# Performance work log

Measured on AMD Instinct MI355X. Metric: run time of the kernel, lower is better.

Reference implementation:

```python
import jax, jax.numpy as jnp
import numpy as np

BN_EPS = 1e-5
TAU = 1.0  # gumbel temperature

def setup_inputs() -> dict:
    key = jax.random.key(0)
    ks = jax.random.split(key, 6)
    B, O, F, H, HID = 32, 4096, 256, 8, 128
    x = jax.random.normal(ks[0], (B, O, F), dtype=jnp.float32)
    gumbel_noise = jax.random.gumbel(ks[1], (B, O, H), dtype=jnp.float32)
    W_in = jax.random.normal(ks[2], (F, HID), dtype=jnp.float32) * (1.0 / np.sqrt(F))
    b_in = jnp.zeros((HID,), jnp.float32)
    W_blk = jax.random.normal(ks[3], (HID, HID), dtype=jnp.float32) * (1.0 / np.sqrt(HID))
    b_blk = jnp.zeros((HID,), jnp.float32)
    bn_gamma = jnp.ones((HID,), jnp.float32)
    bn_beta = jnp.zeros((HID,), jnp.float32)
    W_fc = jax.random.normal(ks[4], (HID, H), dtype=jnp.float32) * (1.0 / np.sqrt(HID))
    b_fc = jnp.zeros((H,), jnp.float32)
    return {"x": x, "gumbel_noise": gumbel_noise, "W_in": W_in, "b_in": b_in,
            "W_blk": W_blk, "b_blk": b_blk, "bn_gamma": bn_gamma, "bn_beta": bn_beta,
            "W_fc": W_fc, "b_fc": b_fc}

def reference(x, gumbel_noise, W_in, b_in, W_blk, b_blk, bn_gamma, bn_beta, W_fc, b_fc):
    B, O, F = x.shape
    xf = x.reshape(B * O, F)
    # DynamicNetwork head: input linear + relu, one residual block (Linear+BN+ReLU), fc
    h = jax.nn.relu(xf @ W_in + b_in)  # (B*O, HID)
    z = h @ W_blk + b_blk
    mu = z.mean(axis=0)
    var = z.var(axis=0)  # biased var, matches BatchNorm training normalization
    z = (z - mu) * jax.lax.rsqrt(var + BN_EPS) * bn_gamma + bn_beta
    h = jax.nn.relu(z) + h  # residual
    logits = (h @ W_fc + b_fc).reshape(B, O, -1)  # (B, O, H)
    # mask out zero-norm observations
    mask = (jnp.linalg.norm(x, axis=2) != 0)[..., None].astype(x.dtype)  # (B, O, 1)
    logits = logits * mask
    # gumbel softmax over observation dim (soft)
    w = jax.nn.softmax((logits + gumbel_noise) / TAU, axis=1)  # (B, O, H)
    # weighted sum pooling: algebraically the repeat-multiply-sum in the original
    pooled = jnp.einsum('boh,bof->bhf', w, x)  # (B, H, F)
    return pooled.reshape(B, -1)  # (B, H*F)
```

## Files before the change

kernel.cpp:

```cpp
#include <hip/hip_runtime.h>
#include <math.h>

#define MB_ 131072
#define F_  256
#define HID_ 128
#define H_  8
#define O_  4096
#define B_  32

typedef __attribute__((ext_vector_type(8))) short short8;
typedef __attribute__((ext_vector_type(4))) float f32x4;

static __device__ __forceinline__ unsigned short f2bf(float f) {
    unsigned int u = __float_as_uint(f);
    unsigned int r = (u + 0x7fffu + ((u >> 16) & 1u)) >> 16;
    return (unsigned short)r;
}
static __device__ __forceinline__ float bflo(unsigned int u) {
    return __uint_as_float(u << 16);
}
static __device__ __forceinline__ float bfhi(unsigned int u) {
    return __uint_as_float(u & 0xffff0000u);
}
static __device__ __forceinline__ unsigned int fkey(float f) {
    unsigned int u = __float_as_uint(f);
    return (u & 0x80000000u) ? ~u : (u | 0x80000000u);
}

__global__ __launch_bounds__(256) void k_prep(
    const float* __restrict__ W_in, const float* __restrict__ W_blk,
    unsigned short* __restrict__ WinT, unsigned short* __restrict__ WblkT,
    unsigned int* __restrict__ Mmax)
{
    const int idx = blockIdx.x * 256 + threadIdx.x;
    if (idx < 256) Mmax[idx] = 0u;
    if (idx < 32768) {
        const int n = idx >> 8, k = idx & 255;
        WinT[idx] = f2bf(W_in[(size_t)k * HID_ + n]);
    } else {
        const int i2 = idx - 32768;
        const int n = i2 >> 7, k = i2 & 127;
        WblkT[i2] = f2bf(W_blk[(size_t)k * HID_ + n]);
    }
}

__global__ __launch_bounds__(512, 4) void k_fused(
    const float* __restrict__ x, const unsigned short* __restrict__ WinT,
    const float* __restrict__ b_in,
    const unsigned short* __restrict__ WblkT, const float* __restrict__ b_blk,
    unsigned short* __restrict__ h_out, unsigned short* __restrict__ z_out,
    float* __restrict__ mask_out,
    float* __restrict__ sumP, float* __restrict__ sumsqP)
{
    __shared__ unsigned short smem[128 * 144];
    __shared__ float msum_s[128];
    __shared__ float csum_s[128], csumsq_s[128];
    unsigned short* a_s = smem;
    unsigned short* b_s = smem + 128 * 72;

    const int tid = threadIdx.x;
    const int R0 = blockIdx.x * 128;
    const int sr = tid >> 2;
    const int sc = tid & 3;
    const int wave = tid >> 6;
    const int wrow = wave >> 2;
    const int wcol = wave & 3;
    const int lane = tid & 63;
    const int lm = lane & 15, quad = lane >> 4;

    if (tid < 128) { msum_s[tid] = 0.f; csum_s[tid] = 0.f; csumsq_s[tid] = 0.f; }
    float ms = 0.f;

    f32x4 acc[4][2];
#pragma unroll
    for (int i = 0; i < 4; i++)
#pragma unroll
        for (int j = 0; j < 2; j++) acc[i][j] = (f32x4){0.f, 0.f, 0.f, 0.f};

    float4 ax[4];
    short8 bxr[2];
#pragma unroll
    for (int q = 0; q < 4; q++)
        ax[q] = *(const float4*)(x + (size_t)(R0 + sr) * F_ + (q * 4 + sc) * 4);
#pragma unroll
    for (int q = 0; q < 2; q++)
        bxr[q] = *(const short8*)(WinT + (size_t)sr * F_ + (sc + 4 * q) * 8);

#pragma unroll
    for (int kt = 0; kt < 4; kt++) {
#pragma unroll
        for (int q = 0; q < 4; q++) {
            const float4 v = ax[q];
            ms += v.x * v.x + v.y * v.y + v.z * v.z + v.w * v.w;
            ushort4 o;
            o.x = f2bf(v.x); o.y = f2bf(v.y); o.z = f2bf(v.z); o.w = f2bf(v.w);
            *(ushort4*)(&a_s[sr * 72 + (q * 4 + sc) * 4]) = o;
        }
#pragma unroll
        for (int q = 0; q < 2; q++)
            *(short8*)(&b_s[sr * 72 + (sc + 4 * q) * 8]) = bxr[q];
        __syncthreads();

        if (kt < 3) {
#pragma unroll
            for (int q = 0; q < 4; q++)
                ax[q] = *(const float4*)(x + (size_t)(R0 + sr) * F_ + (kt + 1) * 64 + (q * 4 + sc) * 4);
#pragma unroll
            for (int q = 0; q < 2; q++)
                bxr[q] = *(const short8*)(WinT + (size_t)sr * F_ + (kt + 1) * 64 + (sc + 4 * q) * 8);
        }

#pragma unroll
        for (int ks = 0; ks < 2; ks++) {
            short8 af[4], bfr[2];
#pragma unroll
            for (int mi = 0; mi < 4; mi++)
                af[mi] = *(const short8*)(&a_s[(wrow * 64 + mi * 16 + lm) * 72 + ks * 32 + quad * 8]);
#pragma unroll
            for (int ni = 0; ni < 2; ni++)
                bfr[ni] = *(const short8*)(&b_s[(wcol * 32 + ni * 16 + lm) * 72 + ks * 32 + quad * 8]);
#pragma unroll
            for (int mi = 0; mi < 4; mi++)
#pragma unroll
                for (int ni = 0; ni < 2; ni++)
                    acc[mi][ni] = __builtin_amdgcn_mfma_f32_16x16x32_bf16(af[mi], bfr[ni], acc[mi][ni], 0, 0, 0);
        }
        __syncthreads();
    }

    atomicAdd(&msum_s[sr], ms);

    short8 wb[4][2];
#pragma unroll
    for (int kt2 = 0; kt2 < 4; kt2++)
#pragma unroll
        for (int ni = 0; ni < 2; ni++)
            wb[kt2][ni] = *(const short8*)(WblkT + (size_t)(wcol * 32 + ni * 16 + lm) * HID_ + kt2 * 32 + quad * 8);

    {
        float bcol[2];
#pragma unroll
        for (int ni = 0; ni < 2; ni++) bcol[ni] = b_in[wcol * 32 + ni * 16 + lm];
#pragma unroll
        for (int mi = 0; mi < 4; mi++)
#pragma unroll
            for (int r = 0; r < 4; r++) {
                const int rl = wrow * 64 + mi * 16 + quad * 4 + r;
                const size_t grow = (size_t)(R0 + rl) * HID_;
#pragma unroll
                for (int ni = 0; ni < 2; ni++) {
                    const int col = wcol * 32 + ni * 16 + lm;
                    const float v = fmaxf(acc[mi][ni][r] + bcol[ni], 0.f);
                    const unsigned short us = f2bf(v);
                    h_out[grow + col] = us;
                    smem[rl * 136 + col] = us;
                }
            }
    }
#pragma unroll
    for (int i = 0; i < 4; i++)
#pragma unroll
        for (int j = 0; j < 2; j++) acc[i][j] = (f32x4){0.f, 0.f, 0.f, 0.f};
    __syncthreads();

    if (tid < 128) mask_out[R0 + tid] = (msum_s[tid] != 0.f) ? 1.f : 0.f;

#pragma unroll
    for (int kt2 = 0; kt2 < 4; kt2++) {
        short8 haf[4];
#pragma unroll
        for (int mi = 0; mi < 4; mi++)
            haf[mi] = *(const short8*)(&smem[(wrow * 64 + mi * 16 + lm) * 136 + kt2 * 32 + quad * 8]);
#pragma unroll
        for (int mi = 0; mi < 4; mi++)
#pragma unroll
            for (int ni = 0; ni < 2; ni++)
                acc[mi][ni] = __builtin_amdgcn_mfma_f32_16x16x32_bf16(haf[mi], wb[kt2][ni], acc[mi][ni], 0, 0, 0);
    }

    float bcol2[2];
#pragma unroll
    for (int ni = 0; ni < 2; ni++) bcol2[ni] = b_blk[wcol * 32 + ni * 16 + lm];
    float s_c[2] = {0.f, 0.f}, ss_c[2] = {0.f, 0.f};
#pragma unroll
    for (int mi = 0; mi < 4; mi++)
#pragma unroll
        for (int r = 0; r < 4; r++) {
            const size_t row = (size_t)R0 + wrow * 64 + mi * 16 + quad * 4 + r;
#pragma unroll
            for (int ni = 0; ni < 2; ni++) {
                const float zv = acc[mi][ni][r] + bcol2[ni];
                s_c[ni] += zv;
                ss_c[ni] += zv * zv;
                z_out[row * HID_ + wcol * 32 + ni * 16 + lm] = f2bf(zv);
            }
        }
#pragma unroll
    for (int ni = 0; ni < 2; ni++) {
        atomicAdd(&csum_s[wcol * 32 + ni * 16 + lm], s_c[ni]);
        atomicAdd(&csumsq_s[wcol * 32 + ni * 16 + lm], ss_c[ni]);
    }
    __syncthreads();
    if (tid < 128) {
        sumP[(size_t)blockIdx.x * 128 + tid] = csum_s[tid];
        sumsqP[(size_t)blockIdx.x * 128 + tid] = csumsq_s[tid];
    }
}

__global__ __launch_bounds__(256) void k_bnfin(
    const float* __restrict__ sumP, const float* __restrict__ sumsqP,
    const float* __restrict__ gamma, const float* __restrict__ beta,
    float* __restrict__ scale, float* __restrict__ shift)
{
    const int c = blockIdx.x;
    const int tid = threadIdx.x;
    float s = 0.f, ss = 0.f;
    for (int i = tid; i < 1024; i += 256) {
        s  += sumP[(size_t)i * 128 + c];
        ss += sumsqP[(size_t)i * 128 + c];
    }
#pragma unroll
    for (int off = 32; off; off >>= 1) {
        s  += __shfl_xor(s, off, 64);
        ss += __shfl_xor(ss, off, 64);
    }
    __shared__ float rs[4], rss[4];
    const int wid = tid >> 6, lane = tid & 63;
    if (lane == 0) { rs[wid] = s; rss[wid] = ss; }
    __syncthreads();
    if (tid == 0) {
        const float S  = rs[0] + rs[1] + rs[2] + rs[3];
        const float SS = rss[0] + rss[1] + rss[2] + rss[3];
        const float inv_m = 1.0f / (float)MB_;
        const float mu = S * inv_m;
        const float var = SS * inv_m - mu * mu;
        const float sc = gamma[c] * rsqrtf(var + 1e-5f);
        scale[c] = sc;
        shift[c] = beta[c] - mu * sc;
    }
}

__global__ __launch_bounds__(256) void k_logits(
    const unsigned short* __restrict__ h_in, const unsigned short* __restrict__ z_in,
    const float* __restrict__ scale, const float* __restrict__ shift,
    const float* __restrict__ W_fc, const float* __restrict__ b_fc,
    const float* __restrict__ mask, const float* __restrict__ gumbel,
    float* __restrict__ t_out, unsigned int* __restrict__ Mmax)
{
    __shared__ float wfc_s[1024];
    __shared__ float sc_s[128], sh_s[128];
    const int tid = threadIdx.x;
    for (int i = tid; i < 1024; i += 256) wfc_s[i] = W_fc[i];
    if (tid < 128) { sc_s[tid] = scale[tid]; sh_s[tid] = shift[tid]; }
    __syncthreads();

    const size_t row0 = (size_t)blockIdx.x * 512 + tid;
    const size_t row1 = row0 + 256;
    float a0[8], a1[8];
#pragma unroll
    for (int j = 0; j < 8; j++) { a0[j] = 0.f; a1[j] = 0.f; }

    const uint4* hp0 = (const uint4*)(h_in + row0 * HID_);
    const uint4* zq0 = (const uint4*)(z_in + row0 * HID_);
    const uint4* hp1 = (const uint4*)(h_in + row1 * HID_);
    const uint4* zq1 = (const uint4*)(z_in + row1 * HID_);

#pragma unroll 2
    for (int kc = 0; kc < 16; kc++) {
        const uint4 h0 = hp0[kc], z0 = zq0[kc];
        const uint4 h1 = hp1[kc], z1 = zq1[kc];
        const unsigned int hs0[4] = {h0.x, h0.y, h0.z, h0.w};
        const unsigned int zs0[4] = {z0.x, z0.y, z0.z, z0.w};
        const unsigned int hs1[4] = {h1.x, h1.y, h1.z, h1.w};
        const unsigned int zs1[4] = {z1.x, z1.y, z1.z, z1.w};
#pragma unroll
        for (int p = 0; p < 4; p++) {
            const int k = kc * 8 + p * 2;
            const float sck0 = sc_s[k], shk0 = sh_s[k];
            const float sck1 = sc_s[k + 1], shk1 = sh_s[k + 1];
            const float4 wA = *(const float4*)&wfc_s[k * 8];
            const float4 wB = *(const float4*)&wfc_s[k * 8 + 4];
            const float4 wC = *(const float4*)&wfc_s[k * 8 + 8];
            const float4 wD = *(const float4*)&wfc_s[k * 8 + 12];
            {
                const float hf0 = bflo(hs0[p]), hf1 = bfhi(hs0[p]);
                const float zf0 = bflo(zs0[p]), zf1 = bfhi(zs0[p]);
                const float hb0 = fmaxf(zf0 * sck0 + shk0, 0.f) + hf0;
                const float hb1 = fmaxf(zf1 * sck1 + shk1, 0.f) + hf1;
                a0[0] += hb0 * wA.x + hb1 * wC.x;  a0[1] += hb0 * wA.y + hb1 * wC.y;
                a0[2] += hb0 * wA.z + hb1 * wC.z;  a0[3] += hb0 * wA.w + hb1 * wC.w;
                a0[4] += hb0 * wB.x + hb1 * wD.x;  a0[5] += hb0 * wB.y + hb1 * wD.y;
                a0[6] += hb0 * wB.z + hb1 * wD.z;  a0[7] += hb0 * wB.w + hb1 * wD.w;
            }
            {
                const float hf0 = bflo(hs1[p]), hf1 = bfhi(hs1[p]);
                const float zf0 = bflo(zs1[p]), zf1 = bfhi(zs1[p]);
                const float hb0 = fmaxf(zf0 * sck0 + shk0, 0.f) + hf0;
                const float hb1 = fmaxf(zf1 * sck1 + shk1, 0.f) + hf1;
                a1[0] += hb0 * wA.x + hb1 * wC.x;  a1[1] += hb0 * wA.y + hb1 * wC.y;
                a1[2] += hb0 * wA.z + hb1 * wC.z;  a1[3] += hb0 * wA.w + hb1 * wC.w;
                a1[4] += hb0 * wB.x + hb1 * wD.x;  a1[5] += hb0 * wB.y + hb1 * wD.y;
                a1[6] += hb0 * wB.z + hb1 * wD.z;  a1[7] += hb0 * wB.w + hb1 * wD.w;
            }
        }
    }

    float bf[8];
#pragma unroll
    for (int j = 0; j < 8; j++) bf[j] = b_fc[j];
    const float mk0 = mask[row0], mk1 = mask[row1];
    float g0[8], g1[8];
    *(float4*)&g0[0] = *(const float4*)(gumbel + row0 * 8);
    *(float4*)&g0[4] = *(const float4*)(gumbel + row0 * 8 + 4);
    *(float4*)&g1[0] = *(const float4*)(gumbel + row1 * 8);
    *(float4*)&g1[4] = *(const float4*)(gumbel + row1 * 8 + 4);
    float t0[8], t1[8];
#pragma unroll
    for (int j = 0; j < 8; j++) {
        t0[j] = (a0[j] + bf[j]) * mk0 + g0[j];
        t1[j] = (a1[j] + bf[j]) * mk1 + g1[j];
    }
    *(float4*)(t_out + row0 * 8)     = *(float4*)&t0[0];
    *(float4*)(t_out + row0 * 8 + 4) = *(float4*)&t0[4];
    *(float4*)(t_out + row1 * 8)     = *(float4*)&t1[0];
    *(float4*)(t_out + row1 * 8 + 4) = *(float4*)&t1[4];

    float tm[8];
#pragma unroll
    for (int j = 0; j < 8; j++) tm[j] = fmaxf(t0[j], t1[j]);
#pragma unroll
    for (int off = 32; off; off >>= 1)
#pragma unroll
        for (int j = 0; j < 8; j++) tm[j] = fmaxf(tm[j], __shfl_xor(tm[j], off, 64));
    if ((tid & 63) == 0) {
        const int bb = blockIdx.x >> 3;
#pragma unroll
        for (int j = 0; j < 8; j++) atomicMax(&Mmax[bb * 8 + j], fkey(tm[j]));
    }
}

__global__ __launch_bounds__(256) void k_pool(
    const float* __restrict__ x, const float* __restrict__ t_in,
    const unsigned int* __restrict__ Mmax,
    float* __restrict__ pp, float* __restrict__ zp)
{
    __shared__ float ws_s[8][64];
    __shared__ float M_s[8];
    const int tid = threadIdx.x;
    const int oc = blockIdx.x;
    const int b  = blockIdx.y;
    if (tid < 8) {
        const unsigned int k = Mmax[b * 8 + tid];
        const unsigned int s = (k & 0x80000000u) ? (k & 0x7fffffffu) : ~k;
        M_s[tid] = __uint_as_float(s);
    }
    __syncthreads();
#pragma unroll
    for (int i = tid; i < 512; i += 256) {
        const int ol = i >> 3, hh = i & 7;
        const float tv = t_in[((size_t)b * O_ + oc * 64 + ol) * H_ + hh];
        ws_s[hh][ol] = __expf(tv - M_s[hh]);
    }
    __syncthreads();
    if (tid < 8) {
        float s = 0.f;
        for (int o = 0; o < 64; o++) s += ws_s[tid][o];
        zp[((size_t)oc * 32 + b) * 8 + tid] = s;
    }
    float acc[8];
#pragma unroll
    for (int hh = 0; hh < 8; hh++) acc[hh] = 0.f;
    const float* xp = x + ((size_t)b * O_ + oc * 64) * F_ + tid;
#pragma unroll 4
    for (int o = 0; o < 64; o++) {
        const float xv = xp[(size_t)o * F_];
#pragma unroll
        for (int hh = 0; hh < 8; hh++) acc[hh] += ws_s[hh][o] * xv;
    }
    float* outp = pp + ((size_t)oc * 32 + b) * 2048;
#pragma unroll
    for (int hh = 0; hh < 8; hh++) outp[hh * 256 + tid] = acc[hh];
}

__global__ __launch_bounds__(256) void k_reduce(
    const float* __restrict__ pp, const float* __restrict__ zp,
    float* __restrict__ out)
{
    const int blk = blockIdx.x;
    const int b = blk >> 3, hh = blk & 7;
    const int tid = threadIdx.x;
    __shared__ float invZ_s;
    if (tid < 64) {
        float z = zp[((size_t)tid * 32 + b) * 8 + hh];
#pragma unroll
        for (int off = 32; off; off >>= 1) z += __shfl_xor(z, off, 64);
        if (tid == 0) invZ_s = 1.f / z;
    }
    __syncthreads();
    float s = 0.f;
    const float* p0 = pp + (size_t)b * 2048 + hh * 256 + tid;
#pragma unroll 8
    for (int ocq = 0; ocq < 64; ocq++) s += p0[(size_t)ocq * 65536];
    out[(size_t)b * 2048 + hh * 256 + tid] = s * invZ_s;
}

extern "C" void kernel_launch(void* const* d_in, const int* in_sizes, int n_in,
                              void* d_out, int out_size, void* d_ws, size_t ws_size,
                              hipStream_t stream)
{
    const float* x      = (const float*)d_in[0];
    const float* gumbel = (const float*)d_in[1];
    const float* W_in   = (const float*)d_in[2];
    const float* b_in   = (const float*)d_in[3];
    const float* W_blk  = (const float*)d_in[4];
    const float* b_blk  = (const float*)d_in[5];
    const float* gamma  = (const float*)d_in[6];
    const float* beta   = (const float*)d_in[7];
    const float* W_fc   = (const float*)d_in[8];
    const float* b_fc   = (const float*)d_in[9];
    float* out = (float*)d_out;
    char* ws = (char*)d_ws;

    unsigned short* h_bf  = (unsigned short*)(ws + 0);
    float* pp     = (float*)(ws + 0);
    float* zp     = (float*)(ws + 16777216);
    unsigned short* z_bf  = (unsigned short*)(ws + 33554432);
    float* mask   = (float*)(ws + 67108864);
    float* sumP   = (float*)(ws + 67633152);
    float* sumsqP = (float*)(ws + 68157440);
    float* scale  = (float*)(ws + 68681728);
    float* shift  = (float*)(ws + 68682240);
    float* t_buf  = (float*)(ws + 68682752);
    unsigned int* Mmax = (unsigned int*)(ws + 72877056);
    unsigned short* WinT  = (unsigned short*)(ws + 72878080);
    unsigned short* WblkT = (unsigned short*)(ws + 72943616);

    k_prep<<<192, 256, 0, stream>>>(W_in, W_blk, WinT, WblkT, Mmax);
    k_fused<<<1024, 512, 0, stream>>>(x, WinT, b_in, WblkT, b_blk, h_bf, z_bf, mask, sumP, sumsqP);
    k_bnfin<<<128, 256, 0, stream>>>(sumP, sumsqP, gamma, beta, scale, shift);
    k_logits<<<256, 256, 0, stream>>>(h_bf, z_bf, scale, shift, W_fc, b_fc, mask, gumbel, t_buf, Mmax);
    k_pool<<<dim3(64, 32), 256, 0, stream>>>(x, t_buf, Mmax, pp, zp);
    k_reduce<<<256, 256, 0, stream>>>(pp, zp, out);
}
```

Before: 303.6 us.

## Load GEMM1 MFMA operands directly from global memory, bypassing LDS staging

The first GEMM (x @ W_in) now has each lane load its MFMA A and B fragments straight from global memory into registers, converting to bf16 in registers, instead of staging tiles through shared memory with syncthreads per k-tile. The k loop is split into 8 steps of 32 with register double-buffering. This removes the LDS write/read traffic and barriers. In exchange, each of the 4 column waves reloads the same x rows from global/L2 (4x redundant x reads), and the per-lane accesses are less coalesced (8 contiguous floats per lane).

```diff
diff --git a/kernel.cpp b/kernel.cpp
--- a/kernel.cpp
+++ b/kernel.cpp
@@ -25,6 +25,15 @@
 static __device__ __forceinline__ unsigned int fkey(float f) {
     unsigned int u = __float_as_uint(f);
     return (u & 0x80000000u) ? ~u : (u | 0x80000000u);
+}
+
+static __device__ __forceinline__ short8 pack_bf16x8(const float4 a, const float4 b) {
+    short8 r;
+    r[0] = (short)f2bf(a.x); r[1] = (short)f2bf(a.y);
+    r[2] = (short)f2bf(a.z); r[3] = (short)f2bf(a.w);
+    r[4] = (short)f2bf(b.x); r[5] = (short)f2bf(b.y);
+    r[6] = (short)f2bf(b.z); r[7] = (short)f2bf(b.w);
+    return r;
 }
 
 __global__ __launch_bounds__(256) void k_prep(
@@ -52,16 +61,12 @@
     float* __restrict__ mask_out,
     float* __restrict__ sumP, float* __restrict__ sumsqP)
 {
-    __shared__ unsigned short smem[128 * 144];
+    __shared__ unsigned short h_s[128 * 136];
     __shared__ float msum_s[128];
     __shared__ float csum_s[128], csumsq_s[128];
-    unsigned short* a_s = smem;
-    unsigned short* b_s = smem + 128 * 72;
 
     const int tid = threadIdx.x;
     const int R0 = blockIdx.x * 128;
-    const int sr = tid >> 2;
-    const int sc = tid & 3;
     const int wave = tid >> 6;
     const int wrow = wave >> 2;
     const int wcol = wave & 3;
@@ -69,66 +74,77 @@
     const int lm = lane & 15, quad = lane >> 4;
 
     if (tid < 128) { msum_s[tid] = 0.f; csum_s[tid] = 0.f; csumsq_s[tid] = 0.f; }
-    float ms = 0.f;
+
+    const float* xr[4];
+#pragma unroll
+    for (int mi = 0; mi < 4; mi++)
+        xr[mi] = x + (size_t)(R0 + wrow * 64 + mi * 16 + lm) * F_ + quad * 8;
+    const unsigned short* wr[2];
+#pragma unroll
+    for (int ni = 0; ni < 2; ni++)
+        wr[ni] = WinT + (size_t)(wcol * 32 + ni * 16 + lm) * F_ + quad * 8;
 
     f32x4 acc[4][2];
 #pragma unroll
     for (int i = 0; i < 4; i++)
 #pragma unroll
         for (int j = 0; j < 2; j++) acc[i][j] = (f32x4){0.f, 0.f, 0.f, 0.f};
-
-    float4 ax[4];
-    short8 bxr[2];
-#pragma unroll
-    for (int q = 0; q < 4; q++)
-        ax[q] = *(const float4*)(x + (size_t)(R0 + sr) * F_ + (q * 4 + sc) * 4);
-#pragma unroll
-    for (int q = 0; q < 2; q++)
-        bxr[q] = *(const short8*)(WinT + (size_t)sr * F_ + (sc + 4 * q) * 8);
-
-#pragma unroll
-    for (int kt = 0; kt < 4; kt++) {
-#pragma unroll
-        for (int q = 0; q < 4; q++) {
-            const float4 v = ax[q];
-            ms += v.x * v.x + v.y * v.y + v.z * v.z + v.w * v.w;
-            ushort4 o;
-            o.x = f2bf(v.x); o.y = f2bf(v.y); o.z = f2bf(v.z); o.w = f2bf(v.w);
-            *(ushort4*)(&a_s[sr * 72 + (q * 4 + sc) * 4]) = o;
+    float ms[4] = {0.f, 0.f, 0.f, 0.f};
+
+    float4 aC[4][2];
+    short8 bC[2];
+#pragma unroll
+    for (int mi = 0; mi < 4; mi++) {
+        aC[mi][0] = *(const float4*)(xr[mi]);
+        aC[mi][1] = *(const float4*)(xr[mi] + 4);
+    }
+#pragma unroll
+    for (int ni = 0; ni < 2; ni++)
+        bC[ni] = *(const short8*)(wr[ni]);
+
+    __syncthreads();
+
+#pragma unroll
+    for (int kt = 0; kt < 8; kt++) {
+        float4 aN[4][2];
+        short8 bN[2];
+        if (kt < 7) {
+#pragma unroll
+            for (int mi = 0; mi < 4; mi++) {
+                aN[mi][0] = *(const float4*)(xr[mi] + (kt + 1) * 32);
+                aN[mi][1] = *(const float4*)(xr[mi] + (kt + 1) * 32 + 4);
+            }
+#pragma unroll
+            for (int ni = 0; ni < 2; ni++)
+                bN[ni] = *(const short8*)(wr[ni] + (kt + 1) * 32);
         }
-#pragma unroll
-        for (int q = 0; q < 2; q++)
-            *(short8*)(&b_s[sr * 72 + (sc + 4 * q) * 8]) = bxr[q];
-        __syncthreads();
-
-        if (kt < 3) {
-#pragma unroll
-            for (int q = 0; q < 4; q++)
-                ax[q] = *(const float4*)(x + (size_t)(R0 + sr) * F_ + (kt + 1) * 64 + (q * 4 + sc) * 4);
-#pragma unroll
-            for (int q = 0; q < 2; q++)
-                bxr[q] = *(const short8*)(WinT + (size_t)sr * F_ + (kt + 1) * 64 + (sc + 4 * q) * 8);
+        short8 af[4];
+#pragma unroll
+        for (int mi = 0; mi < 4; mi++) {
+            const float4 u = aC[mi][0], v = aC[mi][1];
+            if (wcol == 0)
+                ms[mi] += u.x * u.x + u.y * u.y + u.z * u.z + u.w * u.w
+                        + v.x * v.x + v.y * v.y + v.z * v.z + v.w * v.w;
+            af[mi] = pack_bf16x8(u, v);
         }
-
-#pragma unroll
-        for (int ks = 0; ks < 2; ks++) {
-            short8 af[4], bfr[2];
-#pragma unroll
-            for (int mi = 0; mi < 4; mi++)
-                af[mi] = *(const short8*)(&a_s[(wrow * 64 + mi * 16 + lm) * 72 + ks * 32 + quad * 8]);
+#pragma unroll
+        for (int mi = 0; mi < 4; mi++)
 #pragma unroll
             for (int ni = 0; ni < 2; ni++)
-                bfr[ni] = *(const short8*)(&b_s[(wcol * 32 + ni * 16 + lm) * 72 + ks * 32 + quad * 8]);
-#pragma unroll
-            for (int mi = 0; mi < 4; mi++)
-#pragma unroll
-                for (int ni = 0; ni < 2; ni++)
-                    acc[mi][ni] = __builtin_amdgcn_mfma_f32_16x16x32_bf16(af[mi], bfr[ni], acc[mi][ni], 0, 0, 0);
+                acc[mi][ni] = __builtin_amdgcn_mfma_f32_16x16x32_bf16(af[mi], bC[ni], acc[mi][ni], 0, 0, 0);
+        if (kt < 7) {
+#pragma unroll
+            for (int mi = 0; mi < 4; mi++) { aC[mi][0] = aN[mi][0]; aC[mi][1] = aN[mi][1]; }
+#pragma unroll
+            for (int ni = 0; ni < 2; ni++) bC[ni] = bN[ni];
         }
-        __syncthreads();
-    }
-
-    atomicAdd(&msum_s[sr], ms);
+    }
+
+    if (wcol == 0) {
+#pragma unroll
+        for (int mi = 0; mi < 4; mi++)
+            atomicAdd(&msum_s[wrow * 64 + mi * 16 + lm], ms[mi]);
+    }
 
     short8 wb[4][2];
 #pragma unroll
@@ -153,7 +169,7 @@
                     const float v = fmaxf(acc[mi][ni][r] + bcol[ni], 0.f);
                     const unsigned short us = f2bf(v);
                     h_out[grow + col] = us;
-                    smem[rl * 136 + col] = us;
+                    h_s[rl * 136 + col] = us;
                 }
             }
     }
@@ -170,7 +186,7 @@
         short8 haf[4];
 #pragma unroll
         for (int mi = 0; mi < 4; mi++)
-            haf[mi] = *(const short8*)(&smem[(wrow * 64 + mi * 16 + lm) * 136 + kt2 * 32 + quad * 8]);
+            haf[mi] = *(const short8*)(&h_s[(wrow * 64 + mi * 16 + lm) * 136 + kt2 * 32 + quad * 8]);
 #pragma unroll
         for (int mi = 0; mi < 4; mi++)
 #pragma unroll
```

Measured after the change: 361.6 us. +19.1%, slower.
